# Performance work log

Hardware: AMD Instinct MI355X
Metric: run time of the kernel (lower is better)

The kernel has to match this reference:

```python
import jax, jax.numpy as jnp
import numpy as np
from jax import lax

H = 64   # hidden_size
IN = 18  # input_size
L = 4    # lstm_layers
OUT = 3  # output_size
B = 2048
T = 512


def _lstm_layer(x, W_ih, W_hh, b_ih, b_hh):
    # x: [B,T,D]; PyTorch gate order: i, f, g, o
    xg = jnp.einsum('btd,gd->btg', x, W_ih) + b_ih + b_hh  # [B,T,4H]

    def step(carry, xg_t):
        h, c = carry
        gates = xg_t + h @ W_hh.T
        i, f, g, o = jnp.split(gates, 4, axis=-1)
        c = jax.nn.sigmoid(f) * c + jax.nn.sigmoid(i) * jnp.tanh(g)
        h = jax.nn.sigmoid(o) * jnp.tanh(c)
        return (h, c), h

    h0 = jnp.zeros((x.shape[0], H), x.dtype)
    _, hs = lax.scan(step, (h0, h0), jnp.swapaxes(xg, 0, 1))  # hs: [T,B,H]
    return jnp.swapaxes(hs, 0, 1)  # [B,T,H]


def _forward(x, Wi0, Wh0, bi0, bh0, Wi1, Wh1, bi1, bh1,
             Wi2, Wh2, bi2, bh2, Wi3, Wh3, bi3, bh3, W1, b1, W2, b2):
    h = x
    layers = [(Wi0, Wh0, bi0, bh0), (Wi1, Wh1, bi1, bh1),
              (Wi2, Wh2, bi2, bh2), (Wi3, Wh3, bi3, bh3)]
    for Wi, Wh, bi, bh in layers:
        h = _lstm_layer(h, Wi, Wh, bi, bh)
    last = h[:, -1, :]                      # [B,H]
    hid = jax.nn.relu(last @ W1.T + b1)     # [B,128]
    return hid @ W2.T + b2                  # [B,OUT]


def setup_inputs():
    key = jax.random.key(0)
    ks = jax.random.split(key, 1 + 4 * L + 4)
    d = {'x': jax.random.normal(ks[0], (B, T, IN), jnp.float32)}
    k = 1
    s = 0.1
    for l in range(L):
        din = IN if l == 0 else H
        d[f'Wi{l}'] = jax.random.normal(ks[k], (4 * H, din), jnp.float32) * s; k += 1
        d[f'Wh{l}'] = jax.random.normal(ks[k], (4 * H, H), jnp.float32) * s; k += 1
        d[f'bi{l}'] = jax.random.normal(ks[k], (4 * H,), jnp.float32) * s; k += 1
        d[f'bh{l}'] = jax.random.normal(ks[k], (4 * H,), jnp.float32) * s; k += 1
    d['W1'] = jax.random.normal(ks[k], (128, H), jnp.float32) * s; k += 1
    d['b1'] = jax.random.normal(ks[k], (128,), jnp.float32) * s; k += 1
    d['W2'] = jax.random.normal(ks[k], (OUT, 128), jnp.float32) * s; k += 1
    d['b2'] = jax.random.normal(ks[k], (OUT,), jnp.float32) * s
    return d


def reference(x, Wi0, Wh0, bi0, bh0, Wi1, Wh1, bi1, bh1,
              Wi2, Wh2, bi2, bh2, Wi3, Wh3, bi3, bh3, W1, b1, W2, b2):
    return _forward(x, Wi0, Wh0, bi0, bh0, Wi1, Wh1, bi1, bh1,
                    Wi2, Wh2, bi2, bh2, Wi3, Wh3, bi3, bh3, W1, b1, W2, b2)
```

## Files before the change

### kernel.cpp

```cpp
#include <hip/hip_runtime.h>
#include <stdint.h>

typedef __bf16 bf16_t;
typedef __bf16 bf16x8 __attribute__((ext_vector_type(8)));
typedef float  f32x4  __attribute__((ext_vector_type(4)));

union Frag { uint32_t u[4]; bf16x8 v; };

struct WPtrs {
    const float* Wi[4];
    const float* Wh[4];
    const float* bi[4];
    const float* bh[4];
};

#define LOG2E 1.44269504088896340736f

__device__ __forceinline__ float sigm2(float xs) {
    return __builtin_amdgcn_rcpf(1.0f + __builtin_amdgcn_exp2f(-xs));
}
__device__ __forceinline__ float tanh2(float ys) {
    return 1.0f - 2.0f * __builtin_amdgcn_rcpf(__builtin_amdgcn_exp2f(ys) + 1.0f);
}
__device__ __forceinline__ float tanhc(float c) {
    return tanh2(c * (2.0f * LOG2E));
}

__device__ __forceinline__ float dpp_halfswap(float x) {
    int i = __float_as_int(x);
    int r = __builtin_amdgcn_update_dpp(i, i, 0x128 , 0xF, 0xF, false);
    return __int_as_float(r);
}

__global__ __launch_bounds__(1024, 4)
void lstm_fused(const float* __restrict__ x0, float* __restrict__ last_out, WPtrs wp)
{
    const int tile = blockIdx.x;
    const int tid  = threadIdx.x;
    const int w    = tid >> 6;
    const int lane = tid & 63;
    const int l15  = lane & 15;
    const int l4   = lane >> 4;
    const int l    = w >> 2;
    const int uq   = w & 3;
    const bool hiH = (l15 >= 8);
    const int  col = l15 & 7;

    __shared__ uint2 lds_h[2][4][4][64];

    for (int i = tid; i < 2 * 4 * 4 * 64; i += 1024)
        ((uint2*)lds_h)[i] = make_uint2(0u, 0u);

    const float* Wi = wp.Wi[l];
    const float* Wh = wp.Wh[l];

    const float gs[4] = {LOG2E, LOG2E, 2.0f * LOG2E, LOG2E};

    bf16x8 whA[4][2];
    bf16x8 wiA[4][2];
#pragma unroll
    for (int G = 0; G < 4; ++G) {
        const float sc = gs[G];
        const int row = G * 64 + 16 * uq + l15;
        const float* r = Wh + (size_t)row * 64;
#pragma unroll
        for (int s = 0; s < 2; ++s) {
            f32x4 a = *(const f32x4*)(r + 32 * s + 4 * l4);
            f32x4 b = *(const f32x4*)(r + 32 * s + 4 * l4 + 16);
            bf16x8 f;
            f[0] = (bf16_t)(a[0] * sc); f[1] = (bf16_t)(a[1] * sc);
            f[2] = (bf16_t)(a[2] * sc); f[3] = (bf16_t)(a[3] * sc);
            f[4] = (bf16_t)(b[0] * sc); f[5] = (bf16_t)(b[1] * sc);
            f[6] = (bf16_t)(b[2] * sc); f[7] = (bf16_t)(b[3] * sc);
            whA[G][s] = f;
        }
        if (l == 0) {
            const float* ri = Wi + (size_t)row * 18;
            const int k0 = 4 * l4;
            bf16x8 f;
            f[0] = (bf16_t)(ri[k0 + 0] * sc); f[1] = (bf16_t)(ri[k0 + 1] * sc);
            f[2] = (bf16_t)(ri[k0 + 2] * sc); f[3] = (bf16_t)(ri[k0 + 3] * sc);
            f[4] = (l4 == 0) ? (bf16_t)(ri[16] * sc) : (bf16_t)0.0f;
            f[5] = (l4 == 0) ? (bf16_t)(ri[17] * sc) : (bf16_t)0.0f;
            f[6] = (bf16_t)0.0f; f[7] = (bf16_t)0.0f;
            wiA[G][0] = f;
            wiA[G][1] = f;
        } else {
            const float* ri = Wi + (size_t)row * 64;
#pragma unroll
            for (int s = 0; s < 2; ++s) {
                f32x4 a = *(const f32x4*)(ri + 32 * s + 4 * l4);
                f32x4 b = *(const f32x4*)(ri + 32 * s + 4 * l4 + 16);
                bf16x8 f;
                f[0] = (bf16_t)(a[0] * sc); f[1] = (bf16_t)(a[1] * sc);
                f[2] = (bf16_t)(a[2] * sc); f[3] = (bf16_t)(a[3] * sc);
                f[4] = (bf16_t)(b[0] * sc); f[5] = (bf16_t)(b[1] * sc);
                f[6] = (bf16_t)(b[2] * sc); f[7] = (bf16_t)(b[3] * sc);
                wiA[G][s] = f;
            }
        }
    }

    float biasA[4], biasB[4];
#pragma unroll
    for (int G = 0; G < 4; ++G) {
        const int rb = G * 64 + 16 * uq + 4 * l4 + (hiH ? 2 : 0);
        biasA[G] = (wp.bi[l][rb]     + wp.bh[l][rb])     * gs[G];
        biasB[G] = (wp.bi[l][rb + 1] + wp.bh[l][rb + 1]) * gs[G];
    }

    bf16x8& xfA = wiA[2][1];
    bf16x8& xfB = wiA[3][1];
    const int    xbatch = tile * 8 + (hiH ? 7 : col);
    const float* xrow   = x0 + (size_t)xbatch * (512 * 18);
    auto loadx = [&](int t, bf16x8& dst) {
        const float* xr = xrow + t * 18;
        const int k0 = 4 * l4;
        bf16x8 f;
        f[0] = (bf16_t)xr[k0 + 0]; f[1] = (bf16_t)xr[k0 + 1];
        f[2] = (bf16_t)xr[k0 + 2]; f[3] = (bf16_t)xr[k0 + 3];
        f[4] = (l4 == 0) ? (bf16_t)xr[16] : (bf16_t)0.0f;
        f[5] = (l4 == 0) ? (bf16_t)xr[17] : (bf16_t)0.0f;
        f[6] = (bf16_t)0.0f; f[7] = (bf16_t)0.0f;
        dst = f;
    };
    if (l == 0) { loadx(0, xfA); loadx(1, xfB); }

    float c0 = 0.0f, c1 = 0.0f;

    __syncthreads();

    auto phase = [&](int p, bf16x8& xf) {
        const int t = p - l;
        if (t >= 0 && t < 512) {
            const int br = (p & 1) ^ 1;
            const int bw = p & 1;

            const f32x4 z4 = {0.0f, 0.0f, 0.0f, 0.0f};
            f32x4 acc[4];

            if (l == 0) {
#pragma unroll
                for (int G = 0; G < 4; ++G)
                    acc[G] = __builtin_amdgcn_mfma_f32_16x16x32_bf16(wiA[G][0], xf, z4, 0, 0, 0);
                const int tn = (t + 2 < 512) ? t + 2 : t;
                loadx(tn, xf);
            } else {
                uint2 lo = lds_h[br][l - 1][0][lane];
                uint2 hi = lds_h[br][l - 1][1][lane];
                Frag b0; b0.u[0] = lo.x; b0.u[1] = lo.y; b0.u[2] = hi.x; b0.u[3] = hi.y;
#pragma unroll
                for (int G = 0; G < 4; ++G)
                    acc[G] = __builtin_amdgcn_mfma_f32_16x16x32_bf16(wiA[G][0], b0.v, z4, 0, 0, 0);
                lo = lds_h[br][l - 1][2][lane];
                hi = lds_h[br][l - 1][3][lane];
                Frag b1; b1.u[0] = lo.x; b1.u[1] = lo.y; b1.u[2] = hi.x; b1.u[3] = hi.y;
#pragma unroll
                for (int G = 0; G < 4; ++G)
                    acc[G] = __builtin_amdgcn_mfma_f32_16x16x32_bf16(wiA[G][1], b1.v, acc[G], 0, 0, 0);
            }

            {
                uint2 lo = lds_h[br][l][0][lane];
                uint2 hi = lds_h[br][l][1][lane];
                Frag b0; b0.u[0] = lo.x; b0.u[1] = lo.y; b0.u[2] = hi.x; b0.u[3] = hi.y;
#pragma unroll
                for (int G = 0; G < 4; ++G)
                    acc[G] = __builtin_amdgcn_mfma_f32_16x16x32_bf16(whA[G][0], b0.v, acc[G], 0, 0, 0);
                lo = lds_h[br][l][2][lane];
                hi = lds_h[br][l][3][lane];
                Frag b1; b1.u[0] = lo.x; b1.u[1] = lo.y; b1.u[2] = hi.x; b1.u[3] = hi.y;
#pragma unroll
                for (int G = 0; G < 4; ++G)
                    acc[G] = __builtin_amdgcn_mfma_f32_16x16x32_bf16(whA[G][1], b1.v, acc[G], 0, 0, 0);
            }

            float g0[4], g1[4];
#pragma unroll
            for (int G = 0; G < 4; ++G) {
                const float s2 = dpp_halfswap(acc[G][2]);
                const float s3 = dpp_halfswap(acc[G][3]);
                g0[G] = (hiH ? s2 : acc[G][0]) + biasA[G];
                g1[G] = (hiH ? s3 : acc[G][1]) + biasB[G];
            }

            const float cA = sigm2(g0[1]) * c0 + sigm2(g0[0]) * tanh2(g0[2]);
            const float cB = sigm2(g1[1]) * c1 + sigm2(g1[0]) * tanh2(g1[2]);
            c0 = cA; c1 = cB;
            const float hA = sigm2(g0[3]) * tanhc(cA);
            const float hB = sigm2(g1[3]) * tanhc(cB);

            union { uint32_t u; bf16_t b[2]; } pk;
            pk.b[0] = (bf16_t)hA; pk.b[1] = (bf16_t)hB;
            uint32_t* slot = (uint32_t*)&lds_h[bw][l][uq][16 * l4 + col];
            slot[hiH ? 1 : 0] = pk.u;

            if (l == 3 && t == 511) {
                float* o = last_out + ((size_t)(tile * 8 + col)) * 64
                           + 16 * uq + 4 * l4 + (hiH ? 2 : 0);
                *(float2*)o = make_float2(hA, hB);
            }
        }
        __syncthreads();
    };

    for (int p = 0; p < 516; p += 2) {
        phase(p,     xfA);
        phase(p + 1, xfB);
    }
}

__global__ __launch_bounds__(256)
void mlp_head(const float* __restrict__ last,
              const float* __restrict__ W1, const float* __restrict__ b1,
              const float* __restrict__ W2, const float* __restrict__ b2,
              float* __restrict__ out)
{
    __shared__ float sW1[128 * 64];
    __shared__ float sb1[128];
    __shared__ float sW2[3 * 128];
    __shared__ float sb2[4];
    const int tid = threadIdx.x;
    for (int i = tid; i < 128 * 64; i += 256) sW1[i] = W1[i];
    for (int i = tid; i < 128; i += 256) sb1[i] = b1[i];
    for (int i = tid; i < 3 * 128; i += 256) sW2[i] = W2[i];
    if (tid < 3) sb2[tid] = b2[tid];
    __syncthreads();

    const int b = blockIdx.x * 256 + tid;
    const float* lb = last + (size_t)b * 64;
    float xv[64];
#pragma unroll
    for (int k = 0; k < 64; k += 4) {
        f32x4 v = *(const f32x4*)(lb + k);
        xv[k] = v[0]; xv[k + 1] = v[1]; xv[k + 2] = v[2]; xv[k + 3] = v[3];
    }
    float o0 = sb2[0], o1 = sb2[1], o2 = sb2[2];
    for (int j = 0; j < 128; ++j) {
        float a = sb1[j];
        const float* wr = &sW1[j * 64];
#pragma unroll
        for (int k = 0; k < 64; k += 4) {
            f32x4 wv = *(const f32x4*)(wr + k);
            a += xv[k] * wv[0] + xv[k + 1] * wv[1] + xv[k + 2] * wv[2] + xv[k + 3] * wv[3];
        }
        a = fmaxf(a, 0.0f);
        o0 += a * sW2[0 * 128 + j];
        o1 += a * sW2[1 * 128 + j];
        o2 += a * sW2[2 * 128 + j];
    }
    out[(size_t)b * 3 + 0] = o0;
    out[(size_t)b * 3 + 1] = o1;
    out[(size_t)b * 3 + 2] = o2;
}

extern "C" void kernel_launch(void* const* d_in, const int* in_sizes, int n_in,
                              void* d_out, int out_size, void* d_ws, size_t ws_size,
                              hipStream_t stream)
{
    (void)in_sizes; (void)n_in; (void)out_size; (void)ws_size;

    const float* x = (const float*)d_in[0];
    WPtrs wp;
    for (int l = 0; l < 4; ++l) {
        wp.Wi[l] = (const float*)d_in[1 + 4 * l + 0];
        wp.Wh[l] = (const float*)d_in[1 + 4 * l + 1];
        wp.bi[l] = (const float*)d_in[1 + 4 * l + 2];
        wp.bh[l] = (const float*)d_in[1 + 4 * l + 3];
    }
    const float* W1 = (const float*)d_in[17];
    const float* b1 = (const float*)d_in[18];
    const float* W2 = (const float*)d_in[19];
    const float* b2 = (const float*)d_in[20];

    float* last = (float*)d_ws;

    lstm_fused<<<dim3(256), dim3(1024), 0, stream>>>(x, last, wp);
    mlp_head<<<dim3(8), dim3(256), 0, stream>>>(last, W1, b1, W2, b2, (float*)d_out);
}
```

Baseline: 599.2 us.

## Merge LSTM gate reciprocals and transpose h LDS layout for 128-bit reads

Rewrites the cell update so each of c and h uses a single reciprocal over a combined denominator instead of separate reciprocals per sigmoid and tanh. The h buffer in shared memory is transposed to [lane][slot] with padding, so each wave fetches its B fragments with two 128-bit LDS reads instead of four 64-bit ones. Buffer indices are now passed as constants. The goal is fewer transcendental and LDS instructions on the serial recurrence path. The combined-denominator form can overflow when exp2 grows large (for example a large c or a strongly negative gate), which risks inf/NaN where the previous form saturated cleanly.

```diff
diff --git a/kernel.cpp b/kernel.cpp
--- a/kernel.cpp
+++ b/kernel.cpp
@@ -16,14 +16,22 @@
 
 #define LOG2E 1.44269504088896340736f
 
-__device__ __forceinline__ float sigm2(float xs) {
-    return __builtin_amdgcn_rcpf(1.0f + __builtin_amdgcn_exp2f(-xs));
-}
-__device__ __forceinline__ float tanh2(float ys) {
-    return 1.0f - 2.0f * __builtin_amdgcn_rcpf(__builtin_amdgcn_exp2f(ys) + 1.0f);
-}
-__device__ __forceinline__ float tanhc(float c) {
-    return tanh2(c * (2.0f * LOG2E));
+__device__ __forceinline__ float cell_c(float gi, float gf, float gg, float c) {
+    const float ef = __builtin_amdgcn_exp2f(-gf);
+    const float ei = __builtin_amdgcn_exp2f(-gi);
+    const float Eg = __builtin_amdgcn_exp2f(gg);
+    const float pf = 1.0f + ef, pi = 1.0f + ei;
+    const float pg = Eg + 1.0f, mg = Eg - 1.0f;
+    const float num = c * pi * pg + mg * pf;
+    const float den = pf * pi * pg;
+    return num * __builtin_amdgcn_rcpf(den);
+}
+__device__ __forceinline__ float cell_h(float go, float c) {
+    const float Ec = __builtin_amdgcn_exp2f(c * (2.0f * LOG2E));
+    const float eo = __builtin_amdgcn_exp2f(-go);
+    const float num = Ec - 1.0f;
+    const float den = (1.0f + eo) * (Ec + 1.0f);
+    return num * __builtin_amdgcn_rcpf(den);
 }
 
 __device__ __forceinline__ float dpp_halfswap(float x) {
@@ -46,9 +54,9 @@
     const bool hiH = (l15 >= 8);
     const int  col = l15 & 7;
 
-    __shared__ uint2 lds_h[2][4][4][64];
-
-    for (int i = tid; i < 2 * 4 * 4 * 64; i += 1024)
+    __shared__ uint2 lds_h[2][4][64][6];
+
+    for (int i = tid; i < 2 * 4 * 64 * 6; i += 1024)
         ((uint2*)lds_h)[i] = make_uint2(0u, 0u);
 
     const float* Wi = wp.Wi[l];
@@ -130,12 +138,9 @@
 
     __syncthreads();
 
-    auto phase = [&](int p, bf16x8& xf) {
+    auto phase = [&](int p, int br, int bw, bf16x8& xf) {
         const int t = p - l;
         if (t >= 0 && t < 512) {
-            const int br = (p & 1) ^ 1;
-            const int bw = p & 1;
-
             const f32x4 z4 = {0.0f, 0.0f, 0.0f, 0.0f};
             f32x4 acc[4];
 
@@ -143,36 +148,35 @@
 #pragma unroll
                 for (int G = 0; G < 4; ++G)
                     acc[G] = __builtin_amdgcn_mfma_f32_16x16x32_bf16(wiA[G][0], xf, z4, 0, 0, 0);
-                const int tn = (t + 2 < 512) ? t + 2 : t;
-                loadx(tn, xf);
+                loadx((t + 2) & 511, xf);
             } else {
-                uint2 lo = lds_h[br][l - 1][0][lane];
-                uint2 hi = lds_h[br][l - 1][1][lane];
-                Frag b0; b0.u[0] = lo.x; b0.u[1] = lo.y; b0.u[2] = hi.x; b0.u[3] = hi.y;
+                Frag b0, b1;
+                {
+                    uint4 q0 = *(const uint4*)&lds_h[br][l - 1][lane][0];
+                    uint4 q1 = *(const uint4*)&lds_h[br][l - 1][lane][2];
+                    b0.u[0] = q0.x; b0.u[1] = q0.y; b0.u[2] = q0.z; b0.u[3] = q0.w;
+                    b1.u[0] = q1.x; b1.u[1] = q1.y; b1.u[2] = q1.z; b1.u[3] = q1.w;
+                }
 #pragma unroll
                 for (int G = 0; G < 4; ++G)
                     acc[G] = __builtin_amdgcn_mfma_f32_16x16x32_bf16(wiA[G][0], b0.v, z4, 0, 0, 0);
-                lo = lds_h[br][l - 1][2][lane];
-                hi = lds_h[br][l - 1][3][lane];
-                Frag b1; b1.u[0] = lo.x; b1.u[1] = lo.y; b1.u[2] = hi.x; b1.u[3] = hi.y;
 #pragma unroll
                 for (int G = 0; G < 4; ++G)
                     acc[G] = __builtin_amdgcn_mfma_f32_16x16x32_bf16(wiA[G][1], b1.v, acc[G], 0, 0, 0);
             }
 
             {
-                uint2 lo = lds_h[br][l][0][lane];
-                uint2 hi = lds_h[br][l][1][lane];
-                Frag b0; b0.u[0] = lo.x; b0.u[1] = lo.y; b0.u[2] = hi.x; b0.u[3] = hi.y;
-#pragma unroll
-                for (int G = 0; G < 4; ++G)
-                    acc[G] = __builtin_amdgcn_mfma_f32_16x16x32_bf16(whA[G][0], b0.v, acc[G], 0, 0, 0);
-                lo = lds_h[br][l][2][lane];
-                hi = lds_h[br][l][3][lane];
-                Frag b1; b1.u[0] = lo.x; b1.u[1] = lo.y; b1.u[2] = hi.x; b1.u[3] = hi.y;
-#pragma unroll
-                for (int G = 0; G < 4; ++G)
-                    acc[G] = __builtin_amdgcn_mfma_f32_16x16x32_bf16(whA[G][1], b1.v, acc[G], 0, 0, 0);
+                Frag h0, h1;
+                uint4 q0 = *(const uint4*)&lds_h[br][l][lane][0];
+                uint4 q1 = *(const uint4*)&lds_h[br][l][lane][2];
+                h0.u[0] = q0.x; h0.u[1] = q0.y; h0.u[2] = q0.z; h0.u[3] = q0.w;
+                h1.u[0] = q1.x; h1.u[1] = q1.y; h1.u[2] = q1.z; h1.u[3] = q1.w;
+#pragma unroll
+                for (int G = 0; G < 4; ++G)
+                    acc[G] = __builtin_amdgcn_mfma_f32_16x16x32_bf16(whA[G][0], h0.v, acc[G], 0, 0, 0);
+#pragma unroll
+                for (int G = 0; G < 4; ++G)
+                    acc[G] = __builtin_amdgcn_mfma_f32_16x16x32_bf16(whA[G][1], h1.v, acc[G], 0, 0, 0);
             }
 
             float g0[4], g1[4];
@@ -184,15 +188,15 @@
                 g1[G] = (hiH ? s3 : acc[G][1]) + biasB[G];
             }
 
-            const float cA = sigm2(g0[1]) * c0 + sigm2(g0[0]) * tanh2(g0[2]);
-            const float cB = sigm2(g1[1]) * c1 + sigm2(g1[0]) * tanh2(g1[2]);
+            const float cA = cell_c(g0[0], g0[1], g0[2], c0);
+            const float cB = cell_c(g1[0], g1[1], g1[2], c1);
             c0 = cA; c1 = cB;
-            const float hA = sigm2(g0[3]) * tanhc(cA);
-            const float hB = sigm2(g1[3]) * tanhc(cB);
+            const float hA = cell_h(g0[3], cA);
+            const float hB = cell_h(g1[3], cB);
 
             union { uint32_t u; bf16_t b[2]; } pk;
             pk.b[0] = (bf16_t)hA; pk.b[1] = (bf16_t)hB;
-            uint32_t* slot = (uint32_t*)&lds_h[bw][l][uq][16 * l4 + col];
+            uint32_t* slot = (uint32_t*)&lds_h[bw][l][16 * l4 + col][uq];
             slot[hiH ? 1 : 0] = pk.u;
 
             if (l == 3 && t == 511) {
@@ -205,8 +209,8 @@
     };
 
     for (int p = 0; p < 516; p += 2) {
-        phase(p,     xfA);
-        phase(p + 1, xfB);
+        phase(p,     1, 0, xfA);
+        phase(p + 1, 0, 1, xfB);
     }
 }
 
```

After: 581.4 us, median of 2. -3.0%, faster.
